# Kernel tuning notes

Hardware: AMD Instinct MI355X
Metric: run time of the kernel (lower is better)

The kernel has to match this reference:

```python
import jax, jax.numpy as jnp
import numpy as np

H = 2880      # hidden_size
NH = 64       # num query heads
NKV = 8       # num kv heads
D = 64        # head_dim
G = NH // NKV # GQA group size
W = 128       # sliding window (keys per query, incl. self)
THETA = 150000.0
N = 1024      # tokens


def setup_inputs() -> dict:
    key = jax.random.key(0)
    k0, k1, k2, k3 = jax.random.split(key, 4)
    hidden_states = jax.random.normal(k0, (N, H), jnp.float32)
    Wqkv = jax.random.normal(k1, (H, (NH + 2 * NKV) * D), jnp.float32) * (H ** -0.5)
    Wo = jax.random.normal(k2, (NH * D, H), jnp.float32) * ((NH * D) ** -0.5)
    sinks = jax.random.normal(k3, (NH,), jnp.float32)
    positions = jnp.arange(N, dtype=jnp.int64)
    return {"hidden_states": hidden_states, "Wqkv": Wqkv, "Wo": Wo,
            "sinks": sinks, "positions": positions}


def _rope(x, pos):
    # NeoX-style rotary over full head_dim. x: [n, h, D], pos: [n]
    half = D // 2
    inv_freq = 1.0 / (THETA ** (jnp.arange(half, dtype=jnp.float32) / half))
    ang = pos[:, None].astype(jnp.float32) * inv_freq          # [n, half]
    cos = jnp.cos(ang)[:, None, :]
    sin = jnp.sin(ang)[:, None, :]
    x1, x2 = x[..., :half], x[..., half:]
    return jnp.concatenate([x1 * cos - x2 * sin, x2 * cos + x1 * sin], axis=-1)


def reference(hidden_states, Wqkv, Wo, sinks, positions):
    n = hidden_states.shape[0]
    qkv = hidden_states @ Wqkv
    q, k, v = jnp.split(qkv, [NH * D, NH * D + NKV * D], axis=-1)
    q = _rope(q.reshape(n, NH, D), positions)   # [n, NH, D]
    k = _rope(k.reshape(n, NKV, D), positions)  # [n, NKV, D]
    v = v.reshape(n, NKV, D)

    # Sliding-window key indices: query i attends keys j in [i-W+1, i]
    idx = positions[:, None] - (W - 1) + jnp.arange(W)[None, :]  # [n, W]
    valid = idx >= 0
    idx = jnp.clip(idx, 0, n - 1)
    k_win = k[idx]  # [n, W, NKV, D]
    v_win = v[idx]  # [n, W, NKV, D]

    qg = q.reshape(n, NKV, G, D)
    scores = jnp.einsum('nkgd,nwkd->nkgw', qg, k_win) * (D ** -0.5)
    scores = jnp.where(valid[:, None, None, :], scores, -jnp.inf)

    # Attention sinks: softmax over [scores, sink_logit]; sink gets no value.
    sink = sinks.reshape(NKV, G)                      # [NKV, G]
    m = jnp.maximum(scores.max(-1), sink[None])       # [n, NKV, G]
    p = jnp.exp(scores - m[..., None])                # [n, NKV, G, W]
    denom = p.sum(-1) + jnp.exp(sink[None] - m)       # [n, NKV, G]
    out = jnp.einsum('nkgw,nwkd->nkgd', p, v_win) / denom[..., None]
    return out.reshape(n, NH * D) @ Wo
```

## Files before the change

### kernel.cpp

```cpp
#include <hip/hip_runtime.h>
#include <hip/hip_bf16.h>

#define HDIM   2880
#define NH     64
#define NKV    8
#define DHEAD  64
#define GQ     (NH / NKV)
#define WIN    128
#define NTOK   1024
#define QKV_N  ((NH + 2 * NKV) * DHEAD)
#define QCOLS  (NH * DHEAD)
#define KOFF   QCOLS
#define VOFF   (QCOLS + NKV * DHEAD)
#define WO_PAD 2944
#define SK1    3
#define SK2    4

typedef __attribute__((ext_vector_type(8))) short short8;
typedef __attribute__((ext_vector_type(4))) float floatx4;

__device__ unsigned short g_Xb   [(size_t)NTOK  * HDIM];
__device__ unsigned short g_qkvb [(size_t)NTOK  * QKV_N];
__device__ unsigned short g_attn [(size_t)NTOK  * QCOLS];
__device__ unsigned short g_WqkvT[(size_t)QKV_N * HDIM];
__device__ unsigned short g_WoT  [(size_t)WO_PAD * QCOLS];
__device__ float          g_part1[(size_t)SK1 * NTOK * QKV_N];
__device__ float          g_part2[(size_t)SK2 * NTOK * WO_PAD];

__device__ __forceinline__ unsigned short f2b(float f) {
    __hip_bfloat16 h = __float2bfloat16(f);
    return *reinterpret_cast<unsigned short*>(&h);
}

__device__ __forceinline__ void gload_lds16(const unsigned short* g, unsigned short* l) {
    __builtin_amdgcn_global_load_lds(
        (const __attribute__((address_space(1))) unsigned int*)g,
        (__attribute__((address_space(3))) unsigned int*)l, 16, 0, 0);
}

__global__ __launch_bounds__(256) void transpose_cvt(
        const float* __restrict__ in, unsigned short* __restrict__ out,
        int K, int N) {
    int bk = blockIdx.x, bn = blockIdx.y;
    int t = threadIdx.x;
    __shared__ __align__(16) unsigned short T[64 * 72];
    #pragma unroll
    for (int i = 0; i < 4; ++i) {
        int c = i * 256 + t;
        int r = c >> 4, cc = (c & 15) * 4;
        float4 v = *(const float4*)(in + (size_t)(bk * 64 + r) * N + bn * 64 + cc);
        T[r * 72 + cc + 0] = f2b(v.x);
        T[r * 72 + cc + 1] = f2b(v.y);
        T[r * 72 + cc + 2] = f2b(v.z);
        T[r * 72 + cc + 3] = f2b(v.w);
    }
    __syncthreads();
    #pragma unroll
    for (int i = 0; i < 2; ++i) {
        int c = i * 256 + t;
        int rn = c >> 3, kc = (c & 7) * 8;
        int4 vv;
        unsigned short* tp = (unsigned short*)&vv;
        #pragma unroll
        for (int j = 0; j < 8; ++j) tp[j] = T[(kc + j) * 72 + rn];
        *(int4*)(out + (size_t)(bn * 64 + rn) * K + bk * 64 + kc) = vv;
    }
}

__global__ __launch_bounds__(256) void cvt_bf16(
        const float* __restrict__ in, unsigned short* __restrict__ out, int n4) {
    int id = blockIdx.x * 256 + threadIdx.x;
    if (id >= n4) return;
    float4 v = *(const float4*)(in + (size_t)id * 4);
    ushort4 o;
    o.x = f2b(v.x); o.y = f2b(v.y); o.z = f2b(v.z); o.w = f2b(v.w);
    *(ushort4*)(out + (size_t)id * 4) = o;
}

__global__ __launch_bounds__(256) void gemm_sk(
        const unsigned short* __restrict__ A, const unsigned short* __restrict__ Bt,
        float* __restrict__ P, int K, int chunk, int ldc, size_t plane) {
    int bm = blockIdx.x, bn = blockIdx.y, z = blockIdx.z;
    int t = threadIdx.x, lane = t & 63, wid = t >> 6;
    int quad = lane >> 4, ml = lane & 15;
    int wm = wid >> 1, wn = wid & 1;
    __shared__ __align__(16) unsigned short As[128 * 64];
    __shared__ __align__(16) unsigned short Bs[128 * 64];
    floatx4 acc[4][4];
    #pragma unroll
    for (int i = 0; i < 4; ++i)
        #pragma unroll
        for (int j = 0; j < 4; ++j) acc[i][j] = (floatx4){0.f, 0.f, 0.f, 0.f};

    int srow = lane >> 3;
    int scol = (lane & 7) * 8;
    int base = z * chunk;
    const unsigned short* Ab = A  + (size_t)(bm * 128) * K + base;
    const unsigned short* Bb = Bt + (size_t)(bn * 128) * K + base;

    for (int k0 = 0; k0 < chunk; k0 += 64) {
        #pragma unroll
        for (int j = 0; j < 4; ++j) {
            int grp = wid * 4 + j;
            int r = grp * 8 + srow;
            gload_lds16(Ab + (size_t)r * K + k0 + scol, &As[grp * 512]);
            gload_lds16(Bb + (size_t)r * K + k0 + scol, &Bs[grp * 512]);
        }
        __syncthreads();
        #pragma unroll
        for (int kk = 0; kk < 64; kk += 32) {
            short8 af[4], bf[4];
            #pragma unroll
            for (int mt = 0; mt < 4; ++mt)
                af[mt] = *(const short8*)&As[(wm * 64 + mt * 16 + ml) * 64 + kk + quad * 8];
            #pragma unroll
            for (int nt = 0; nt < 4; ++nt)
                bf[nt] = *(const short8*)&Bs[(wn * 64 + nt * 16 + ml) * 64 + kk + quad * 8];
            #pragma unroll
            for (int mt = 0; mt < 4; ++mt)
                #pragma unroll
                for (int nt = 0; nt < 4; ++nt)
                    acc[mt][nt] = __builtin_amdgcn_mfma_f32_16x16x32_bf16(af[mt], bf[nt], acc[mt][nt], 0, 0, 0);
        }
        __syncthreads();
    }
    float* Cp = P + z * plane;
    #pragma unroll
    for (int mt = 0; mt < 4; ++mt)
        #pragma unroll
        for (int nt = 0; nt < 4; ++nt)
            #pragma unroll
            for (int r = 0; r < 4; ++r) {
                int row = bm * 128 + wm * 64 + mt * 16 + quad * 4 + r;
                int col = bn * 128 + wn * 64 + nt * 16 + ml;
                Cp[(size_t)row * ldc + col] = acc[mt][nt][r];
            }
}

#define QK_UNITS (NTOK * 72 * 8)
#define V_UNITS  (NTOK * 128)
__global__ __launch_bounds__(256) void reduce_rope(
        const float* __restrict__ P, unsigned short* __restrict__ qkvb) {
    int id = blockIdx.x * 256 + threadIdx.x;
    const size_t plane = (size_t)NTOK * QKV_N;
    if (id < QK_UNITS) {
        int n = id / 576;
        int rem = id - n * 576;
        int hh = rem >> 3, q8 = rem & 7;
        int c0 = (hh < NH) ? hh * 64 : KOFF + (hh - NH) * 64;
        size_t i1 = (size_t)n * QKV_N + c0 + q8 * 4;
        float4 a0 = *(const float4*)(P + i1);
        float4 a1 = *(const float4*)(P + plane + i1);
        float4 a2 = *(const float4*)(P + 2 * plane + i1);
        float4 b0 = *(const float4*)(P + i1 + 32);
        float4 b1 = *(const float4*)(P + plane + i1 + 32);
        float4 b2 = *(const float4*)(P + 2 * plane + i1 + 32);
        float x1[4] = {a0.x + a1.x + a2.x, a0.y + a1.y + a2.y,
                       a0.z + a1.z + a2.z, a0.w + a1.w + a2.w};
        float x2[4] = {b0.x + b1.x + b2.x, b0.y + b1.y + b2.y,
                       b0.z + b1.z + b2.z, b0.w + b1.w + b2.w};
        union { ushort4 v; unsigned short u[4]; } o1, o2;
        #pragma unroll
        for (int j = 0; j < 4; ++j) {
            int d = q8 * 4 + j;
            float inv = expf(-(float)d * 0.3724497053f);
            float ang = (float)n * inv;
            float s, c;
            sincosf(ang, &s, &c);
            o1.u[j] = f2b(x1[j] * c - x2[j] * s);
            o2.u[j] = f2b(x2[j] * c + x1[j] * s);
        }
        *(ushort4*)(qkvb + i1) = o1.v;
        *(ushort4*)(qkvb + i1 + 32) = o2.v;
    } else if (id < QK_UNITS + V_UNITS) {
        int vid = id - QK_UNITS;
        int n = vid >> 7, s8 = vid & 127;
        size_t i1 = (size_t)n * QKV_N + VOFF + s8 * 4;
        float4 a0 = *(const float4*)(P + i1);
        float4 a1 = *(const float4*)(P + plane + i1);
        float4 a2 = *(const float4*)(P + 2 * plane + i1);
        union { ushort4 v; unsigned short u[4]; } o;
        o.u[0] = f2b(a0.x + a1.x + a2.x);
        o.u[1] = f2b(a0.y + a1.y + a2.y);
        o.u[2] = f2b(a0.z + a1.z + a2.z);
        o.u[3] = f2b(a0.w + a1.w + a2.w);
        *(ushort4*)(qkvb + i1) = o.v;
    }
}

__global__ __launch_bounds__(256) void reduce_out(
        const float* __restrict__ P, float* __restrict__ out) {
    int id = blockIdx.x * 256 + threadIdx.x;
    if (id >= NTOK * (HDIM / 4)) return;
    int n = id / (HDIM / 4);
    int c = (id - n * (HDIM / 4)) * 4;
    const size_t plane = (size_t)NTOK * WO_PAD;
    size_t i = (size_t)n * WO_PAD + c;
    float4 a0 = *(const float4*)(P + i);
    float4 a1 = *(const float4*)(P + plane + i);
    float4 a2 = *(const float4*)(P + 2 * plane + i);
    float4 a3 = *(const float4*)(P + 3 * plane + i);
    float4 s;
    s.x = a0.x + a1.x + a2.x + a3.x;
    s.y = a0.y + a1.y + a2.y + a3.y;
    s.z = a0.z + a1.z + a2.z + a3.z;
    s.w = a0.w + a1.w + a2.w + a3.w;
    *(float4*)(out + (size_t)n * HDIM + c) = s;
}

#define TQ     16
#define WROWS  160
#define KS_LD  72
#define VT_LD  168
#define PS_LD  168

__global__ __launch_bounds__(256) void attn_mfma(
        const unsigned short* __restrict__ qkvb,
        const float* __restrict__ sinks,
        unsigned short* __restrict__ aout) {
    int t0 = blockIdx.x * TQ, kh = blockIdx.y;
    int t = threadIdx.x, lane = t & 63, wid = t >> 6;
    int quad = lane >> 4, ml = lane & 15;
    int wavebase = wid * 32;

    __shared__ __align__(16) unsigned short Ks[WROWS * KS_LD];
    __shared__ __align__(16) unsigned short Vt[DHEAD * VT_LD];
    __shared__ __align__(16) unsigned short Ps[4 * 16 * PS_LD];
    unsigned short* Psw = &Ps[wid * 16 * PS_LD];

    #pragma unroll
    for (int i = 0; i < 5; ++i) {
        int c = i * 256 + t;
        int w = c >> 3, d8 = (c & 7) * 8;
        int r = t0 - 127 + w;
        r = min(max(r, 0), NTOK - 1);
        *(int4*)&Ks[w * KS_LD + d8] =
            *(const int4*)(qkvb + (size_t)r * QKV_N + KOFF + kh * DHEAD + d8);
        int4 vv = *(const int4*)(qkvb + (size_t)r * QKV_N + VOFF + kh * DHEAD + d8);
        const unsigned short* vp = (const unsigned short*)&vv;
        #pragma unroll
        for (int j = 0; j < 8; ++j) Vt[(d8 + j) * VT_LD + w] = vp[j];
    }
    __syncthreads();

    short8 qf[2][2];
    #pragma unroll
    for (int mt = 0; mt < 2; ++mt) {
        int m = wavebase + mt * 16 + ml;
        int tl = m & 15, g = m >> 4;
        const unsigned short* qp = qkvb + (size_t)(t0 + tl) * QKV_N + (kh * GQ + g) * DHEAD;
        #pragma unroll
        for (int kk = 0; kk < 2; ++kk)
            qf[mt][kk] = *(const short8*)(qp + kk * 32 + quad * 8);
    }

    floatx4 S[2][10];
    #pragma unroll
    for (int mt = 0; mt < 2; ++mt)
        #pragma unroll
        for (int nt = 0; nt < 10; ++nt) S[mt][nt] = (floatx4){0.f, 0.f, 0.f, 0.f};
    #pragma unroll
    for (int kk = 0; kk < 2; ++kk) {
        #pragma unroll
        for (int nt = 0; nt < 10; ++nt) {
            short8 kb = *(const short8*)&Ks[(nt * 16 + ml) * KS_LD + kk * 32 + quad * 8];
            #pragma unroll
            for (int mt = 0; mt < 2; ++mt)
                S[mt][nt] = __builtin_amdgcn_mfma_f32_16x16x32_bf16(qf[mt][kk], kb, S[mt][nt], 0, 0, 0);
        }
    }

    int wmin0 = 127 - t0;
    #pragma unroll
    for (int mt = 0; mt < 2; ++mt) {
        #pragma unroll
        for (int r = 0; r < 4; ++r) {
            int tl = (wavebase + mt * 16 + quad * 4 + r) & 15;
            int wlo = tl > wmin0 ? tl : wmin0;
            int whi = tl + 127;
            #pragma unroll
            for (int nt = 0; nt < 10; ++nt) {
                int w = nt * 16 + ml;
                float s = S[mt][nt][r] * 0.125f;
                S[mt][nt][r] = (w >= wlo && w <= whi) ? s : -INFINITY;
            }
        }
    }

    #pragma unroll
    for (int mt = 0; mt < 2; ++mt) {
        int g = (wavebase + mt * 16) >> 4;
        float sk = sinks[kh * GQ + g];
        #pragma unroll
        for (int r = 0; r < 4; ++r) {
            float rm = -INFINITY;
            #pragma unroll
            for (int nt = 0; nt < 10; ++nt) rm = fmaxf(rm, S[mt][nt][r]);
            #pragma unroll
            for (int off = 1; off < 16; off <<= 1) rm = fmaxf(rm, __shfl_xor(rm, off));
            rm = fmaxf(rm, sk);
            float sum = 0.f;
            #pragma unroll
            for (int nt = 0; nt < 10; ++nt) {
                float p = __expf(S[mt][nt][r] - rm);
                S[mt][nt][r] = p;
                sum += p;
            }
            #pragma unroll
            for (int off = 1; off < 16; off <<= 1) sum += __shfl_xor(sum, off);
            float inv = 1.f / (sum + __expf(sk - rm));
            #pragma unroll
            for (int nt = 0; nt < 10; ++nt) S[mt][nt][r] *= inv;
        }
    }

    #pragma unroll
    for (int mt = 0; mt < 2; ++mt) {
        #pragma unroll
        for (int r = 0; r < 4; ++r) {
            int lr = quad * 4 + r;
            #pragma unroll
            for (int nt = 0; nt < 10; ++nt)
                Psw[lr * PS_LD + nt * 16 + ml] = f2b(S[mt][nt][r]);
        }
        floatx4 O[4];
        #pragma unroll
        for (int j = 0; j < 4; ++j) O[j] = (floatx4){0.f, 0.f, 0.f, 0.f};
        #pragma unroll
        for (int ks = 0; ks < 5; ++ks) {
            short8 pf = *(const short8*)&Psw[ml * PS_LD + ks * 32 + quad * 8];
            #pragma unroll
            for (int nt = 0; nt < 4; ++nt) {
                short8 vf = *(const short8*)&Vt[(nt * 16 + ml) * VT_LD + ks * 32 + quad * 8];
                O[nt] = __builtin_amdgcn_mfma_f32_16x16x32_bf16(pf, vf, O[nt], 0, 0, 0);
            }
        }
        #pragma unroll
        for (int r = 0; r < 4; ++r) {
            int mm = wavebase + mt * 16 + quad * 4 + r;
            int tl = mm & 15, g = mm >> 4;
            unsigned short* op = aout + (size_t)(t0 + tl) * QCOLS + (kh * GQ + g) * DHEAD;
            #pragma unroll
            for (int nt = 0; nt < 4; ++nt)
                op[nt * 16 + ml] = f2b(O[nt][r]);
        }
    }
}

extern "C" void kernel_launch(void* const* d_in, const int* in_sizes, int n_in,
                              void* d_out, int out_size, void* d_ws, size_t ws_size,
                              hipStream_t stream) {
    const float* X     = (const float*)d_in[0];
    const float* Wqkv  = (const float*)d_in[1];
    const float* Wo    = (const float*)d_in[2];
    const float* sinks = (const float*)d_in[3];
    float* out = (float*)d_out;

    unsigned short *Xb, *qkvb, *attn, *WqkvT, *WoT;
    float *part1, *part2;
    hipGetSymbolAddress((void**)&Xb,    HIP_SYMBOL(g_Xb));
    hipGetSymbolAddress((void**)&qkvb,  HIP_SYMBOL(g_qkvb));
    hipGetSymbolAddress((void**)&attn,  HIP_SYMBOL(g_attn));
    hipGetSymbolAddress((void**)&WqkvT, HIP_SYMBOL(g_WqkvT));
    hipGetSymbolAddress((void**)&WoT,   HIP_SYMBOL(g_WoT));
    hipGetSymbolAddress((void**)&part1, HIP_SYMBOL(g_part1));
    hipGetSymbolAddress((void**)&part2, HIP_SYMBOL(g_part2));

    cvt_bf16<<<(NTOK * HDIM / 4 + 255) / 256, 256, 0, stream>>>(X, Xb, NTOK * HDIM / 4);
    transpose_cvt<<<dim3(HDIM / 64, QKV_N / 64), 256, 0, stream>>>(Wqkv, WqkvT, HDIM, QKV_N);
    transpose_cvt<<<dim3(QCOLS / 64, HDIM / 64), 256, 0, stream>>>(Wo, WoT, QCOLS, HDIM);

    gemm_sk<<<dim3(NTOK / 128, QKV_N / 128, SK1), 256, 0, stream>>>(
        Xb, WqkvT, part1, HDIM, HDIM / SK1, QKV_N, (size_t)NTOK * QKV_N);

    reduce_rope<<<(QK_UNITS + V_UNITS) / 256, 256, 0, stream>>>(part1, qkvb);

    attn_mfma<<<dim3(NTOK / TQ, NKV), 256, 0, stream>>>(qkvb, sinks, attn);

    gemm_sk<<<dim3(NTOK / 128, WO_PAD / 128, SK2), 256, 0, stream>>>(
        attn, WoT, part2, QCOLS, QCOLS / SK2, WO_PAD, (size_t)NTOK * WO_PAD);

    reduce_out<<<(NTOK * (HDIM / 4) + 255) / 256, 256, 0, stream>>>(part2, out);
}
```

Measured before the change: 333.0 us.

## Merge prep kernels, remap GEMM blocks per XCD, restructure V transpose loads

The three conversion/transpose launches are merged into a single prep kernel. Both split-K GEMMs now use a 1D grid whose blocks are remapped so that each XCD handles whole N-column groups across all M tiles and K-splits, to improve L2 reuse of weight tiles on the chiplet-partitioned GPU. WO_PAD grows to 3072 so the N-tile count divides by 8, which adds some padded work. The attention kernel's V load is split into its own loop with a w-major index order, so consecutive threads write adjacent LDS columns during the transpose.

```diff
diff --git a/kernel.cpp b/kernel.cpp
--- a/kernel.cpp
+++ b/kernel.cpp
@@ -12,7 +12,7 @@
 #define QCOLS  (NH * DHEAD)
 #define KOFF   QCOLS
 #define VOFF   (QCOLS + NKV * DHEAD)
-#define WO_PAD 2944
+#define WO_PAD 3072
 #define SK1    3
 #define SK2    4
 
@@ -38,12 +38,34 @@
         (__attribute__((address_space(3))) unsigned int*)l, 16, 0, 0);
 }
 
-__global__ __launch_bounds__(256) void transpose_cvt(
-        const float* __restrict__ in, unsigned short* __restrict__ out,
-        int K, int N) {
-    int bk = blockIdx.x, bn = blockIdx.y;
-    int t = threadIdx.x;
+#define T1_BLKS (45 * 80)
+#define T2_BLKS (64 * 45)
+#define CV_BLKS 2880
+
+__global__ __launch_bounds__(256) void prep(
+        const float* __restrict__ X, const float* __restrict__ Wqkv,
+        const float* __restrict__ Wo, unsigned short* __restrict__ Xb,
+        unsigned short* __restrict__ WqkvT, unsigned short* __restrict__ WoT) {
     __shared__ __align__(16) unsigned short T[64 * 72];
+    int b = blockIdx.x, t = threadIdx.x;
+    const float* in;
+    unsigned short* out;
+    int K, N, bk, bn;
+    if (b < T1_BLKS) {
+        in = Wqkv; out = WqkvT; K = HDIM; N = QKV_N;
+        bk = b % 45; bn = b / 45;
+    } else if (b < T1_BLKS + T2_BLKS) {
+        int b2 = b - T1_BLKS;
+        in = Wo; out = WoT; K = QCOLS; N = HDIM;
+        bk = b2 % 64; bn = b2 / 64;
+    } else {
+        int id = (b - T1_BLKS - T2_BLKS) * 256 + t;
+        float4 v = *(const float4*)(X + (size_t)id * 4);
+        ushort4 o;
+        o.x = f2b(v.x); o.y = f2b(v.y); o.z = f2b(v.z); o.w = f2b(v.w);
+        *(ushort4*)(Xb + (size_t)id * 4) = o;
+        return;
+    }
     #pragma unroll
     for (int i = 0; i < 4; ++i) {
         int c = i * 256 + t;
@@ -67,20 +89,18 @@
     }
 }
 
-__global__ __launch_bounds__(256) void cvt_bf16(
-        const float* __restrict__ in, unsigned short* __restrict__ out, int n4) {
-    int id = blockIdx.x * 256 + threadIdx.x;
-    if (id >= n4) return;
-    float4 v = *(const float4*)(in + (size_t)id * 4);
-    ushort4 o;
-    o.x = f2b(v.x); o.y = f2b(v.y); o.z = f2b(v.z); o.w = f2b(v.w);
-    *(ushort4*)(out + (size_t)id * 4) = o;
-}
-
 __global__ __launch_bounds__(256) void gemm_sk(
         const unsigned short* __restrict__ A, const unsigned short* __restrict__ Bt,
-        float* __restrict__ P, int K, int chunk, int ldc, size_t plane) {
-    int bm = blockIdx.x, bn = blockIdx.y, z = blockIdx.z;
+        float* __restrict__ P, int K, int chunk, int ldc, size_t plane, int sk) {
+    int sk8 = sk << 3;
+    int xcd = blockIdx.x & 7;
+    int idx = blockIdx.x >> 3;
+    int grp = idx / sk8;
+    int rem = idx - grp * sk8;
+    int bn = xcd + (grp << 3);
+    int bm = rem & 7;
+    int z  = rem >> 3;
+
     int t = threadIdx.x, lane = t & 63, wid = t >> 6;
     int quad = lane >> 4, ml = lane & 15;
     int wm = wid >> 1, wn = wid & 1;
@@ -101,10 +121,10 @@
     for (int k0 = 0; k0 < chunk; k0 += 64) {
         #pragma unroll
         for (int j = 0; j < 4; ++j) {
-            int grp = wid * 4 + j;
-            int r = grp * 8 + srow;
-            gload_lds16(Ab + (size_t)r * K + k0 + scol, &As[grp * 512]);
-            gload_lds16(Bb + (size_t)r * K + k0 + scol, &Bs[grp * 512]);
+            int grp8 = wid * 4 + j;
+            int r = grp8 * 8 + srow;
+            gload_lds16(Ab + (size_t)r * K + k0 + scol, &As[grp8 * 512]);
+            gload_lds16(Bb + (size_t)r * K + k0 + scol, &Bs[grp8 * 512]);
         }
         __syncthreads();
         #pragma unroll
@@ -236,6 +256,13 @@
         r = min(max(r, 0), NTOK - 1);
         *(int4*)&Ks[w * KS_LD + d8] =
             *(const int4*)(qkvb + (size_t)r * QKV_N + KOFF + kh * DHEAD + d8);
+    }
+    #pragma unroll
+    for (int i = 0; i < 5; ++i) {
+        int c = i * 256 + t;
+        int w = c % 160, d8 = (c / 160) * 8;
+        int r = t0 - 127 + w;
+        r = min(max(r, 0), NTOK - 1);
         int4 vv = *(const int4*)(qkvb + (size_t)r * QKV_N + VOFF + kh * DHEAD + d8);
         const unsigned short* vp = (const unsigned short*)&vv;
         #pragma unroll
@@ -366,19 +393,17 @@
     hipGetSymbolAddress((void**)&part1, HIP_SYMBOL(g_part1));
     hipGetSymbolAddress((void**)&part2, HIP_SYMBOL(g_part2));
 
-    cvt_bf16<<<(NTOK * HDIM / 4 + 255) / 256, 256, 0, stream>>>(X, Xb, NTOK * HDIM / 4);
-    transpose_cvt<<<dim3(HDIM / 64, QKV_N / 64), 256, 0, stream>>>(Wqkv, WqkvT, HDIM, QKV_N);
-    transpose_cvt<<<dim3(QCOLS / 64, HDIM / 64), 256, 0, stream>>>(Wo, WoT, QCOLS, HDIM);
-
-    gemm_sk<<<dim3(NTOK / 128, QKV_N / 128, SK1), 256, 0, stream>>>(
-        Xb, WqkvT, part1, HDIM, HDIM / SK1, QKV_N, (size_t)NTOK * QKV_N);
+    prep<<<T1_BLKS + T2_BLKS + CV_BLKS, 256, 0, stream>>>(X, Wqkv, Wo, Xb, WqkvT, WoT);
+
+    gemm_sk<<<8 * 5 * 8 * SK1, 256, 0, stream>>>(
+        Xb, WqkvT, part1, HDIM, HDIM / SK1, QKV_N, (size_t)NTOK * QKV_N, SK1);
 
     reduce_rope<<<(QK_UNITS + V_UNITS) / 256, 256, 0, stream>>>(part1, qkvb);
 
     attn_mfma<<<dim3(NTOK / TQ, NKV), 256, 0, stream>>>(qkvb, sinks, attn);
 
-    gemm_sk<<<dim3(NTOK / 128, WO_PAD / 128, SK2), 256, 0, stream>>>(
-        attn, WoT, part2, QCOLS, QCOLS / SK2, WO_PAD, (size_t)NTOK * WO_PAD);
+    gemm_sk<<<8 * 3 * 8 * SK2, 256, 0, stream>>>(
+        attn, WoT, part2, QCOLS, QCOLS / SK2, WO_PAD, (size_t)NTOK * WO_PAD, SK2);
 
     reduce_out<<<(NTOK * (HDIM / 4) + 255) / 256, 256, 0, stream>>>(part2, out);
 }
```

Result: no change. 336.6 us (+1.1%).
